# Optimization experiments

Measured on AMD Instinct MI355X. Metric: run time of the kernel, lower is better.

Reference implementation:

```python
import jax, jax.numpy as jnp
import numpy as np

MAX_SEQ_LEN = 128
ROPE_BASE = 10000.0
D_MODEL = 2048
N_HEADS = 16
D_HEAD = D_MODEL // N_HEADS
B = 64
T = 128


def _rope_caches(d_head, max_seq_len, base=ROPE_BASE):
    thetas = 1.0 / base ** (jnp.arange(0, d_head, 2, dtype=jnp.float32) / d_head)
    freqs = jnp.arange(max_seq_len, dtype=jnp.float32)[:, None] * thetas[None, :]
    return jnp.cos(freqs), jnp.sin(freqs)


def _apply_rope(x, cos, sin):
    # x: (..., T, d_head); cos/sin: (T, d_head/2)
    x_even = x[..., 0::2]
    x_odd = x[..., 1::2]
    rot_even = x_even * cos - x_odd * sin
    rot_odd = x_even * sin + x_odd * cos
    return jnp.stack([rot_even, rot_odd], axis=-1).reshape(x.shape)


def setup_inputs() -> dict:
    key = jax.random.key(0)
    kx, kq, kk, kv, ko = jax.random.split(key, 5)
    s = 1.0 / np.sqrt(D_MODEL)
    x = jax.random.normal(kx, (B, T, D_MODEL), dtype=jnp.float32)
    W_Q = jax.random.normal(kq, (D_MODEL, D_MODEL), dtype=jnp.float32) * s
    W_K = jax.random.normal(kk, (D_MODEL, D_MODEL), dtype=jnp.float32) * s
    W_V = jax.random.normal(kv, (D_MODEL, D_MODEL), dtype=jnp.float32) * s
    W_O = jax.random.normal(ko, (D_MODEL, D_MODEL), dtype=jnp.float32) * s
    mask = jnp.tril(jnp.ones((T, T), dtype=bool))[None, None]  # (1,1,T,T) causal
    return {"x": x, "W_Q": W_Q, "W_K": W_K, "W_V": W_V, "W_O": W_O, "mask": mask}


def reference(x, W_Q, W_K, W_V, W_O, mask):
    Bsz, Tlen, D = x.shape
    cos, sin = _rope_caches(D_HEAD, MAX_SEQ_LEN)
    cos, sin = cos[:Tlen], sin[:Tlen]

    def proj(W):
        # nn.Linear: x @ W.T ; reshape to (B, H, T, d_head)
        return (x @ W.T).reshape(Bsz, Tlen, N_HEADS, D_HEAD).transpose(0, 2, 1, 3)

    Q = _apply_rope(proj(W_Q), cos, sin)
    K = _apply_rope(proj(W_K), cos, sin)
    V = proj(W_V)

    scale = jnp.float32(np.sqrt(D_HEAD))
    scores = jnp.einsum("bhqd,bhkd->bhqk", Q, K) / scale
    scores = jnp.where(mask, scores, -jnp.inf)
    weights = jax.nn.softmax(scores, axis=-1)
    attn = jnp.einsum("bhqk,bhkd->bhqd", weights, V)
    attn = attn.transpose(0, 2, 1, 3).reshape(Bsz, Tlen, D)
    return attn @ W_O.T
```

## Files before the change

kernel.cpp:

```cpp
#include <hip/hip_runtime.h>
#include <hip/hip_bf16.h>
#include <math.h>

#define D_MODEL 2048
#define N_HEADS 16
#define D_HEAD  128
#define BATCH   64
#define SEQ     128
#define BT      (BATCH*SEQ)
#define LDF     6144
#define KOFF    2048
#define VOFF    4096

typedef __bf16 bf16;
typedef __attribute__((ext_vector_type(8))) __bf16 bf16x8;
typedef __attribute__((ext_vector_type(4))) float  f32x4;

__device__ __forceinline__ f32x4 mfma16(bf16x8 a, bf16x8 b, f32x4 c) {
    return __builtin_amdgcn_mfma_f32_16x16x32_bf16(a, b, c, 0, 0, 0);
}

__device__ __forceinline__ bf16x8 cvt8_f32(const float* p) {
    f32x4 lo = *(const f32x4*)p;
    f32x4 hi = *(const f32x4*)(p + 4);
    bf16x8 r;
    r[0] = (bf16)lo[0]; r[1] = (bf16)lo[1]; r[2] = (bf16)lo[2]; r[3] = (bf16)lo[3];
    r[4] = (bf16)hi[0]; r[5] = (bf16)hi[1]; r[6] = (bf16)hi[2]; r[7] = (bf16)hi[3];
    return r;
}

__device__ __forceinline__ void gl2lds16(const bf16* g, bf16* l) {
    __builtin_amdgcn_global_load_lds(
        (const __attribute__((address_space(1))) void*)g,
        (__attribute__((address_space(3))) void*)l, 16, 0, 0);
}

__device__ __forceinline__ bf16x8 rope8(bf16x8 v, int tpos, int pair0) {
    bf16x8 r;
    for (int m = 0; m < 4; ++m) {
        int i = pair0 + m;
        float theta = __expf((float)(2 * i) * (-9.210340371976184f / 128.0f));
        float ang   = (float)tpos * theta;
        float sn, cs;
        __sincosf(ang, &sn, &cs);
        float e = (float)v[2 * m], o = (float)v[2 * m + 1];
        r[2 * m]     = (bf16)(e * cs - o * sn);
        r[2 * m + 1] = (bf16)(e * sn + o * cs);
    }
    return r;
}

__global__ __launch_bounds__(256) void cvt_kernel(const float* __restrict__ src,
                                                  bf16* __restrict__ dst, int n8)
{
    int i = blockIdx.x * 256 + threadIdx.x;
    if (i < n8) *(bf16x8*)(dst + (size_t)i * 8) = cvt8_f32(src + (size_t)i * 8);
}

__global__ __launch_bounds__(256) void cvt_w3(const float* __restrict__ w0,
                                              const float* __restrict__ w1,
                                              const float* __restrict__ w2,
                                              bf16* __restrict__ dst)
{
    int i   = blockIdx.x * 256 + threadIdx.x;
    int sel = i >> 19;
    int off = i & ((1 << 19) - 1);
    const float* s = (sel == 0) ? w0 : (sel == 1) ? w1 : w2;
    *(bf16x8*)(dst + (size_t)i * 8) = cvt8_f32(s + (size_t)off * 8);
}


#define BAR() __builtin_amdgcn_s_barrier()

#define READ_A(BSEL, mh) do {                                                 \
    _Pragma("unroll") for (int ii = 0; ii < 4; ++ii)                          \
    _Pragma("unroll") for (int kk = 0; kk < 2; ++kk)                          \
        Af[ii][kk] = *(const bf16x8*)&As[BSEL][aoff[(mh)*4+ii] + ksw[kk]];    \
    } while (0)

#define READ_B(BSEL, j0) do {                                                 \
    _Pragma("unroll") for (int jj = 0; jj < 2; ++jj)                          \
    _Pragma("unroll") for (int kk = 0; kk < 2; ++kk)                          \
        Bf[(j0)+jj][kk] = *(const bf16x8*)&Bs[BSEL][bof[(j0)+jj] + ksw[kk]];  \
    } while (0)

#define MQ(i0, j0) do {                                                       \
    __builtin_amdgcn_s_setprio(1);                                            \
    _Pragma("unroll") for (int ii = 0; ii < 4; ++ii)                          \
    _Pragma("unroll") for (int jj = 0; jj < 2; ++jj)                          \
    _Pragma("unroll") for (int kk = 0; kk < 2; ++kk)                          \
        acc[(i0)+ii][(j0)+jj] =                                               \
            mfma16(Af[ii][kk], Bf[(j0)+jj][kk], acc[(i0)+ii][(j0)+jj]);       \
    __builtin_amdgcn_s_setprio(0);                                            \
    } while (0)

#define STAGE(BSEL, tt) do {                                                  \
    const size_t _k = (size_t)(tt) * 64;                                      \
    _Pragma("unroll") for (int c = 0; c < 4; ++c) {                           \
        gl2lds16(Ag + (size_t)c * 64 * lda + _k, &As[BSEL][c*4096 + w*512]);  \
        gl2lds16(Bg + (size_t)c * 64 * ldb + _k, &Bs[BSEL][c*4096 + w*512]);  \
    } } while (0)

#define TILE_ITER(BSEL, tt, MODE) do {                                        \
    READ_A(BSEL, 0); READ_B(BSEL, 0); BAR(); MQ(0, 0); BAR();                 \
    READ_B(BSEL, 2);                  BAR(); MQ(0, 2); BAR();                 \
    READ_A(BSEL, 1);                  BAR(); MQ(4, 2);                        \
    __builtin_amdgcn_sched_barrier(0); BAR();                                 \
    if (MODE == 0) STAGE(BSEL, (tt) + 2);                                     \
    BAR(); MQ(4, 0);                                                          \
    if (MODE == 0) asm volatile("s_waitcnt vmcnt(8)" ::: "memory");           \
    if (MODE == 1) asm volatile("s_waitcnt vmcnt(0)" ::: "memory");           \
    BAR(); } while (0)

template<typename OutT>
__global__ __launch_bounds__(512, 2) void gemm256(const bf16* __restrict__ A,
                                                  const bf16* __restrict__ B,
                                                  OutT* __restrict__ C,
                                                  int lda, int ldb, int ldc,
                                                  int K, int gx)
{
    __shared__ __align__(16) bf16 As[2][16384];
    __shared__ __align__(16) bf16 Bs[2][16384];

    const int tid  = threadIdx.x;
    const int w    = tid >> 6;
    const int l    = tid & 63;
    const int quad = l >> 4;
    const int ln   = l & 15;
    const int wm   = w >> 2;
    const int wn   = w & 3;

    const int nwg = gridDim.x;
    const int bid = blockIdx.x;
    const int swz = (bid & 7) * (nwg >> 3) + (bid >> 3);
    const int bx  = swz % gx;
    const int by  = swz / gx;
    const size_t mbase = (size_t)by * 256;
    const size_t nbase = (size_t)bx * 256;

    const int srow   = tid >> 3;
    const int schunk = (tid & 7) ^ (srow & 7);
    const bf16* Ag = A + (mbase + srow) * (size_t)lda + schunk * 8;
    const bf16* Bg = B + (nbase + srow) * (size_t)ldb + schunk * 8;

    const int xr = ln & 7;
    int aoff[8], bof[4], ksw[2];
#pragma unroll
    for (int i = 0; i < 8; ++i) aoff[i] = (wm * 128 + i * 16 + ln) * 64;
#pragma unroll
    for (int j = 0; j < 4; ++j) bof[j]  = (wn * 64  + j * 16 + ln) * 64;
#pragma unroll
    for (int kk = 0; kk < 2; ++kk) ksw[kk] = ((kk * 4 + quad) ^ xr) * 8;

    f32x4 acc[8][4];
#pragma unroll
    for (int i = 0; i < 8; ++i)
#pragma unroll
        for (int j = 0; j < 4; ++j) acc[i][j] = (f32x4){0.f, 0.f, 0.f, 0.f};

    bf16x8 Af[4][2];
    bf16x8 Bf[4][2];

    STAGE(0, 0);
    STAGE(1, 1);
    asm volatile("s_waitcnt vmcnt(8)" ::: "memory");
    BAR();

    const int NT = K >> 6;
    int t = 0;
#pragma unroll 1
    for (; t < NT - 2; t += 2) {
        TILE_ITER(0, t, 0);
        TILE_ITER(1, t + 1, 0);
    }
    TILE_ITER(0, NT - 2, 1);
    TILE_ITER(1, NT - 1, 2);

#pragma unroll
    for (int i = 0; i < 8; ++i)
#pragma unroll
        for (int j = 0; j < 4; ++j)
#pragma unroll
            for (int r = 0; r < 4; ++r) {
                size_t row = mbase + wm * 128 + i * 16 + quad * 4 + r;
                size_t col = nbase + wn * 64 + j * 16 + ln;
                C[row * (size_t)ldc + col] = (OutT)acc[i][j][r];
            }
}

#undef BAR
#undef READ_A
#undef READ_B
#undef MQ
#undef STAGE
#undef TILE_ITER

__global__ __launch_bounds__(256) void attn_kernel(bf16* __restrict__ buf)
{
    __shared__ __align__(16) bf16 KP_lds[128 * 136];
    __shared__ __align__(16) bf16 Vt_lds[128 * 136];

    const int bh = blockIdx.x;
    const int b  = bh >> 4;
    const int h  = bh & 15;
    const size_t baseQ = (size_t)b * SEQ * LDF + (size_t)h * D_HEAD;
    const size_t baseK = baseQ + KOFF;
    const size_t baseV = baseQ + VOFF;

    const int tid  = threadIdx.x;
    const int w    = tid >> 6;
    const int l    = tid & 63;
    const int quad = l >> 4;
    const int ln   = l & 15;

    {
        int k  = tid >> 1;
        int d0 = (tid & 1) * 64;
        const bf16* kp = buf + baseK + (size_t)k * LDF + d0;
        const bf16* vp = buf + baseV + (size_t)k * LDF + d0;
        for (int c = 0; c < 8; ++c) {
            bf16x8 kv = *(const bf16x8*)(kp + c * 8);
            *(bf16x8*)&KP_lds[k * 136 + d0 + c * 8] = rope8(kv, k, d0 / 2 + c * 4);
            bf16x8 vv = *(const bf16x8*)(vp + c * 8);
            for (int j = 0; j < 8; ++j)
                Vt_lds[(d0 + c * 8 + j) * 136 + k] = vv[j];
        }
    }
    __syncthreads();

    const float rscale = 0.08838834764831845f;
    const float NEG    = -1e30f;

    f32x4 acc2[2][8];
    for (int s = 0; s < 2; ++s)
        for (int nt = 0; nt < 8; ++nt) acc2[s][nt] = (f32x4){0.f, 0.f, 0.f, 0.f};

    for (int s = 0; s < 2; ++s) {
        const int q0 = w * 32 + s * 16;
        for (int kt = 0; kt < 4; ++kt) {
            bf16x8 qa = *(const bf16x8*)(buf + baseQ + (size_t)(q0 + ln) * LDF
                                           + kt * 32 + quad * 8);
            bf16x8 a = rope8(qa, q0 + ln, kt * 16 + quad * 4);
            for (int nt = 0; nt < 8; ++nt) {
                bf16x8 bb = *(const bf16x8*)&KP_lds[(nt * 16 + ln) * 136
                                                    + kt * 32 + quad * 8];
                acc2[s][nt] = mfma16(a, bb, acc2[s][nt]);
            }
        }

        float mx[4] = {NEG, NEG, NEG, NEG};
        for (int nt = 0; nt < 8; ++nt)
            for (int r = 0; r < 4; ++r) {
                int q = q0 + quad * 4 + r;
                int c = nt * 16 + ln;
                float v = acc2[s][nt][r] * rscale;
                v = (c <= q) ? v : NEG;
                acc2[s][nt][r] = v;
                mx[r] = fmaxf(mx[r], v);
            }
        for (int m = 1; m < 16; m <<= 1)
            for (int r = 0; r < 4; ++r)
                mx[r] = fmaxf(mx[r], __shfl_xor(mx[r], m));

        float sm[4] = {0.f, 0.f, 0.f, 0.f};
        for (int nt = 0; nt < 8; ++nt)
            for (int r = 0; r < 4; ++r) {
                float p = __expf(acc2[s][nt][r] - mx[r]);
                acc2[s][nt][r] = p;
                sm[r] += p;
            }
        for (int m = 1; m < 16; m <<= 1)
            for (int r = 0; r < 4; ++r)
                sm[r] += __shfl_xor(sm[r], m);

        for (int r = 0; r < 4; ++r) sm[r] = 1.0f / sm[r];
        for (int nt = 0; nt < 8; ++nt)
            for (int r = 0; r < 4; ++r)
                acc2[s][nt][r] *= sm[r];
    }

    __syncthreads();

    for (int s = 0; s < 2; ++s)
        for (int nt = 0; nt < 8; ++nt)
            for (int r = 0; r < 4; ++r) {
                int q = w * 32 + s * 16 + quad * 4 + r;
                int c = nt * 16 + ln;
                KP_lds[q * 136 + c] = (bf16)acc2[s][nt][r];
            }

    f32x4 o[2][8];
    for (int s = 0; s < 2; ++s)
        for (int nt = 0; nt < 8; ++nt) o[s][nt] = (f32x4){0.f, 0.f, 0.f, 0.f};

    for (int kt = 0; kt < 4; ++kt) {
        bf16x8 a0 = *(const bf16x8*)&KP_lds[(w * 32 +      ln) * 136 + kt * 32 + quad * 8];
        bf16x8 a1 = *(const bf16x8*)&KP_lds[(w * 32 + 16 + ln) * 136 + kt * 32 + quad * 8];
        for (int nt = 0; nt < 8; ++nt) {
            bf16x8 bb = *(const bf16x8*)&Vt_lds[(nt * 16 + ln) * 136 + kt * 32 + quad * 8];
            o[0][nt] = mfma16(a0, bb, o[0][nt]);
            o[1][nt] = mfma16(a1, bb, o[1][nt]);
        }
    }

    for (int s = 0; s < 2; ++s)
        for (int nt = 0; nt < 8; ++nt)
            for (int r = 0; r < 4; ++r) {
                int q = w * 32 + s * 16 + quad * 4 + r;
                int d = nt * 16 + ln;
                buf[baseQ + (size_t)q * LDF + d] = (bf16)o[s][nt][r];
            }
}

extern "C" void kernel_launch(void* const* d_in, const int* in_sizes, int n_in,
                              void* d_out, int out_size, void* d_ws, size_t ws_size,
                              hipStream_t stream)
{
    const float* x  = (const float*)d_in[0];
    const float* Wq = (const float*)d_in[1];
    const float* Wk = (const float*)d_in[2];
    const float* Wv = (const float*)d_in[3];
    const float* Wo = (const float*)d_in[4];
    float* out = (float*)d_out;

    bf16* QKV = (bf16*)d_ws;
    bf16* xb  = QKV + (size_t)BT * LDF;
    bf16* WB  = xb + (size_t)BT * D_MODEL;
    bf16* WoB = xb;

    const int n8x = BT * D_MODEL / 8;
    const int n8w = D_MODEL * D_MODEL / 8;

    cvt_kernel<<<(n8x + 255) / 256, 256, 0, stream>>>(x, xb, n8x);
    cvt_w3<<<(3 * n8w) / 256, 256, 0, stream>>>(Wq, Wk, Wv, WB);

    gemm256<bf16><<<dim3((LDF / 256) * (BT / 256)), 512, 0, stream>>>(
        xb, WB, QKV, D_MODEL, D_MODEL, LDF, D_MODEL, LDF / 256);

    cvt_kernel<<<(n8w + 255) / 256, 256, 0, stream>>>(Wo, WoB, n8w);

    attn_kernel<<<BATCH * N_HEADS, 256, 0, stream>>>(QKV);

    gemm256<float><<<dim3((D_MODEL / 256) * (BT / 256)), 512, 0, stream>>>(
        QKV, WoB, out, LDF, D_MODEL, D_MODEL, D_MODEL, D_MODEL / 256);
}
```

Measured before the change: 471.1 us.

## Interleave global-to-LDS staging across MFMA phases of GEMM tile loop

Splits the per-tile bulk stage of 8 global-to-LDS loads into single-chunk loads spread across the four MFMA phases of each tile iteration. The first two chunks of the next-next tile are issued early and the remaining six of the next tile trickle in during compute, so the wait drops to vmcnt(2). Explicit lgkmcnt waits and sched_barriers pin the instruction order. The aim is to smooth memory traffic and hide load latency behind MFMA. The tighter dependency ordering across buffers raises the risk of LDS race or stall errors.

```diff
diff --git a/kernel.cpp b/kernel.cpp
--- a/kernel.cpp
+++ b/kernel.cpp
@@ -71,6 +71,8 @@
 
 
 #define BAR() __builtin_amdgcn_s_barrier()
+#define SB0() __builtin_amdgcn_sched_barrier(0)
+#define WAIT_LGKM0() asm volatile("s_waitcnt lgkmcnt(0)" ::: "memory")
 
 #define READ_A(BSEL, mh) do {                                                 \
     _Pragma("unroll") for (int ii = 0; ii < 4; ++ii)                          \
@@ -94,23 +96,42 @@
     __builtin_amdgcn_s_setprio(0);                                            \
     } while (0)
 
-#define STAGE(BSEL, tt) do {                                                  \
-    const size_t _k = (size_t)(tt) * 64;                                      \
-    _Pragma("unroll") for (int c = 0; c < 4; ++c) {                           \
-        gl2lds16(Ag + (size_t)c * 64 * lda + _k, &As[BSEL][c*4096 + w*512]);  \
-        gl2lds16(Bg + (size_t)c * 64 * ldb + _k, &Bs[BSEL][c*4096 + w*512]);  \
-    } } while (0)
-
-#define TILE_ITER(BSEL, tt, MODE) do {                                        \
-    READ_A(BSEL, 0); READ_B(BSEL, 0); BAR(); MQ(0, 0); BAR();                 \
-    READ_B(BSEL, 2);                  BAR(); MQ(0, 2); BAR();                 \
-    READ_A(BSEL, 1);                  BAR(); MQ(4, 2);                        \
-    __builtin_amdgcn_sched_barrier(0); BAR();                                 \
-    if (MODE == 0) STAGE(BSEL, (tt) + 2);                                     \
-    BAR(); MQ(4, 0);                                                          \
-    if (MODE == 0) asm volatile("s_waitcnt vmcnt(8)" ::: "memory");           \
+#define STG1(BSEL, tt, c) do {                                                \
+    if ((c) < 4)                                                              \
+        gl2lds16(Ag + (size_t)(c) * 64 * lda + (size_t)(tt) * 64,             \
+                 &As[BSEL][(c) * 4096 + w * 512]);                            \
+    else                                                                      \
+        gl2lds16(Bg + (size_t)((c) - 4) * 64 * ldb + (size_t)(tt) * 64,       \
+                 &Bs[BSEL][((c) - 4) * 4096 + w * 512]);                      \
+    } while (0)
+
+#define TILE_ITER(BSEL, OSEL, tt, MODE) do {                                  \
+              \
+    READ_A(BSEL, 0); READ_B(BSEL, 0);                                         \
+    if (MODE < 2) { STG1(OSEL, (tt) + 1, 2); STG1(OSEL, (tt) + 1, 3); }       \
+    asm volatile("s_waitcnt lgkmcnt(8)" ::: "memory");                        \
+    SB0(); BAR(); WAIT_LGKM0(); SB0();                                        \
+    MQ(0, 0);                                                                 \
+    SB0(); BAR();                                                             \
+                            \
+    READ_B(BSEL, 2);                                                          \
+    if (MODE < 2) { STG1(OSEL, (tt) + 1, 4); STG1(OSEL, (tt) + 1, 5); }       \
+    SB0(); BAR(); WAIT_LGKM0(); SB0();                                        \
+    MQ(0, 2);                                                                 \
+    SB0(); BAR();                                                             \
+                        \
+    READ_A(BSEL, 1);                                                          \
+    if (MODE < 2) { STG1(OSEL, (tt) + 1, 6); STG1(OSEL, (tt) + 1, 7); }       \
+    SB0(); BAR(); WAIT_LGKM0(); SB0();                                        \
+    MQ(4, 2);                                                                 \
+    SB0(); BAR();                                                             \
+     \
+    if (MODE == 0) { STG1(BSEL, (tt) + 2, 0); STG1(BSEL, (tt) + 2, 1); }      \
+    SB0(); BAR(); SB0();                                                      \
+    MQ(4, 0);                                                                 \
+    if (MODE == 0) asm volatile("s_waitcnt vmcnt(2)" ::: "memory");           \
     if (MODE == 1) asm volatile("s_waitcnt vmcnt(0)" ::: "memory");           \
-    BAR(); } while (0)
+    SB0(); BAR(); } while (0)
 
 template<typename OutT>
 __global__ __launch_bounds__(512, 2) void gemm256(const bf16* __restrict__ A,
@@ -161,20 +182,21 @@
     bf16x8 Af[4][2];
     bf16x8 Bf[4][2];
 
-    STAGE(0, 0);
-    STAGE(1, 1);
-    asm volatile("s_waitcnt vmcnt(8)" ::: "memory");
+    STG1(0, 0, 0); STG1(0, 0, 1); STG1(0, 0, 2); STG1(0, 0, 3);
+    STG1(0, 0, 4); STG1(0, 0, 5); STG1(0, 0, 6); STG1(0, 0, 7);
+    STG1(1, 1, 0); STG1(1, 1, 1);
+    asm volatile("s_waitcnt vmcnt(2)" ::: "memory");
     BAR();
 
     const int NT = K >> 6;
     int t = 0;
 #pragma unroll 1
     for (; t < NT - 2; t += 2) {
-        TILE_ITER(0, t, 0);
-        TILE_ITER(1, t + 1, 0);
-    }
-    TILE_ITER(0, NT - 2, 1);
-    TILE_ITER(1, NT - 1, 2);
+        TILE_ITER(0, 1, t, 0);
+        TILE_ITER(1, 0, t + 1, 0);
+    }
+    TILE_ITER(0, 1, NT - 2, 1);
+    TILE_ITER(1, 0, NT - 1, 2);
 
 #pragma unroll
     for (int i = 0; i < 8; ++i)
@@ -189,10 +211,12 @@
 }
 
 #undef BAR
+#undef SB0
+#undef WAIT_LGKM0
 #undef READ_A
 #undef READ_B
 #undef MQ
-#undef STAGE
+#undef STG1
 #undef TILE_ITER
 
 __global__ __launch_bounds__(256) void attn_kernel(bf16* __restrict__ buf)
```

Result: faster. 460.6 us (-2.2%).

## Restructure GEMM main loop to double-buffer register fragments per k-half

Applied to the files above, without the earlier changes.

The 256x256 GEMM main loop is rebuilt. Each k-half now loads all A and B fragments (8+4) into double-buffered registers, then issues 32 MFMAs in one block. Global-to-LDS staging of the next tile is issued at the start of each tile with a full vmcnt(0) wait, so the prefetch distance drops from two tiles ahead to one. The goal is fewer barriers per tile and LDS reads overlapping MFMA, at the cost of more fragment registers and less latency hiding for global loads.

```diff
diff --git a/kernel.cpp b/kernel.cpp
--- a/kernel.cpp
+++ b/kernel.cpp
@@ -71,46 +71,48 @@
 
 
 #define BAR() __builtin_amdgcn_s_barrier()
-
-#define READ_A(BSEL, mh) do {                                                 \
-    _Pragma("unroll") for (int ii = 0; ii < 4; ++ii)                          \
-    _Pragma("unroll") for (int kk = 0; kk < 2; ++kk)                          \
-        Af[ii][kk] = *(const bf16x8*)&As[BSEL][aoff[(mh)*4+ii] + ksw[kk]];    \
+#define SB0() __builtin_amdgcn_sched_barrier(0)
+
+#define READS(BSEL, KS, BK) do {                                              \
+    _Pragma("unroll") for (int ii = 0; ii < 8; ++ii)                          \
+        Fa[BK][ii] = *(const bf16x8*)&As[BSEL][aoff[ii] + ksw[KS]];           \
+    _Pragma("unroll") for (int jj = 0; jj < 4; ++jj)                          \
+        Fb[BK][jj] = *(const bf16x8*)&Bs[BSEL][bof[jj] + ksw[KS]];            \
     } while (0)
 
-#define READ_B(BSEL, j0) do {                                                 \
-    _Pragma("unroll") for (int jj = 0; jj < 2; ++jj)                          \
-    _Pragma("unroll") for (int kk = 0; kk < 2; ++kk)                          \
-        Bf[(j0)+jj][kk] = *(const bf16x8*)&Bs[BSEL][bof[(j0)+jj] + ksw[kk]];  \
-    } while (0)
-
-#define MQ(i0, j0) do {                                                       \
+#define MQ32(BK) do {                                                         \
     __builtin_amdgcn_s_setprio(1);                                            \
-    _Pragma("unroll") for (int ii = 0; ii < 4; ++ii)                          \
-    _Pragma("unroll") for (int jj = 0; jj < 2; ++jj)                          \
-    _Pragma("unroll") for (int kk = 0; kk < 2; ++kk)                          \
-        acc[(i0)+ii][(j0)+jj] =                                               \
-            mfma16(Af[ii][kk], Bf[(j0)+jj][kk], acc[(i0)+ii][(j0)+jj]);       \
+    _Pragma("unroll") for (int ii = 0; ii < 8; ++ii)                          \
+    _Pragma("unroll") for (int jj = 0; jj < 4; ++jj)                          \
+        acc[ii][jj] = mfma16(Fa[BK][ii], Fb[BK][jj], acc[ii][jj]);            \
     __builtin_amdgcn_s_setprio(0);                                            \
     } while (0)
 
-#define STAGE(BSEL, tt) do {                                                  \
+#define STAGE8(BSEL, tt) do {                                                 \
     const size_t _k = (size_t)(tt) * 64;                                      \
     _Pragma("unroll") for (int c = 0; c < 4; ++c) {                           \
         gl2lds16(Ag + (size_t)c * 64 * lda + _k, &As[BSEL][c*4096 + w*512]);  \
         gl2lds16(Bg + (size_t)c * 64 * ldb + _k, &Bs[BSEL][c*4096 + w*512]);  \
     } } while (0)
 
-#define TILE_ITER(BSEL, tt, MODE) do {                                        \
-    READ_A(BSEL, 0); READ_B(BSEL, 0); BAR(); MQ(0, 0); BAR();                 \
-    READ_B(BSEL, 2);                  BAR(); MQ(0, 2); BAR();                 \
-    READ_A(BSEL, 1);                  BAR(); MQ(4, 2);                        \
-    __builtin_amdgcn_sched_barrier(0); BAR();                                 \
-    if (MODE == 0) STAGE(BSEL, (tt) + 2);                                     \
-    BAR(); MQ(4, 0);                                                          \
-    if (MODE == 0) asm volatile("s_waitcnt vmcnt(8)" ::: "memory");           \
-    if (MODE == 1) asm volatile("s_waitcnt vmcnt(0)" ::: "memory");           \
-    BAR(); } while (0)
+#define TILE(BSEL, OSEL, tt, MODE) do {                                       \
+     \
+    if (MODE == 0) STAGE8(OSEL, (tt) + 1);                                    \
+    READS(BSEL, 1, 1);                                                        \
+    SB0(); BAR();                                                             \
+    asm volatile("s_waitcnt lgkmcnt(12)" ::: "memory"); SB0();                \
+    MQ32(0);                                                                  \
+    if (MODE == 0) asm volatile("s_waitcnt vmcnt(0)" ::: "memory");           \
+    SB0(); BAR();                                                             \
+            \
+    if (MODE == 0) READS(OSEL, 0, 0);                                         \
+    SB0(); BAR();                                                             \
+    if (MODE == 0) { asm volatile("s_waitcnt lgkmcnt(12)" ::: "memory"); }    \
+    else           { asm volatile("s_waitcnt lgkmcnt(0)"  ::: "memory"); }    \
+    SB0();                                                                    \
+    MQ32(1);                                                                  \
+    SB0(); BAR();                                                             \
+    } while (0)
 
 template<typename OutT>
 __global__ __launch_bounds__(512, 2) void gemm256(const bf16* __restrict__ A,
@@ -158,23 +160,23 @@
 #pragma unroll
         for (int j = 0; j < 4; ++j) acc[i][j] = (f32x4){0.f, 0.f, 0.f, 0.f};
 
-    bf16x8 Af[4][2];
-    bf16x8 Bf[4][2];
-
-    STAGE(0, 0);
-    STAGE(1, 1);
-    asm volatile("s_waitcnt vmcnt(8)" ::: "memory");
+    bf16x8 Fa[2][8];
+    bf16x8 Fb[2][4];
+
+    STAGE8(0, 0);
+    asm volatile("s_waitcnt vmcnt(0)" ::: "memory");
     BAR();
+    READS(0, 0, 0);
 
     const int NT = K >> 6;
     int t = 0;
 #pragma unroll 1
     for (; t < NT - 2; t += 2) {
-        TILE_ITER(0, t, 0);
-        TILE_ITER(1, t + 1, 0);
-    }
-    TILE_ITER(0, NT - 2, 1);
-    TILE_ITER(1, NT - 1, 2);
+        TILE(0, 1, t, 0);
+        TILE(1, 0, t + 1, 0);
+    }
+    TILE(0, 1, NT - 2, 0);
+    TILE(1, 0, NT - 1, 1);
 
 #pragma unroll
     for (int i = 0; i < 8; ++i)
@@ -189,11 +191,11 @@
 }
 
 #undef BAR
-#undef READ_A
-#undef READ_B
-#undef MQ
-#undef STAGE
-#undef TILE_ITER
+#undef SB0
+#undef READS
+#undef MQ32
+#undef STAGE8
+#undef TILE
 
 __global__ __launch_bounds__(256) void attn_kernel(bf16* __restrict__ buf)
 {
```

After: 569.3 us. 20.8% more time.
